# Kernel optimization log

Measured on AMD Instinct MI355X. Metric: run time of the kernel, lower is better.

## Reference

```python
import jax, jax.numpy as jnp
import numpy as np

SCALE = 10000.0
PSF = 21          # psf_h == psf_w == psf_d
PAD = PSF // 2    # 10


def setup_inputs() -> dict:
    key = jax.random.key(0)
    k1, k2, k3, k4, k5, k6, k7 = jax.random.split(key, 7)
    N = 8192
    BS, C, H, W, D = 1, 16, 256, 256, 64
    return {
        "psf_raw": jax.random.normal(k1, (N, 1, PSF, PSF, PSF), dtype=jnp.float32),
        "i_val": jax.random.uniform(k2, (N,), dtype=jnp.float32),
        "b": jax.random.randint(k3, (N,), 0, BS, dtype=jnp.int32),
        "ch": jax.random.randint(k4, (N,), 0, C, dtype=jnp.int32),
        "z": jax.random.randint(k5, (N,), 0, H, dtype=jnp.int32),
        "y": jax.random.randint(k6, (N,), 0, W, dtype=jnp.int32),
        "x": jax.random.randint(k7, (N,), 0, D, dtype=jnp.int32),
        "BS": BS, "C": C, "H": H, "W": W, "D": D,
    }


def reference(psf_raw, i_val, b, ch, z, y, x, BS, C, H, W, D):
    # 1) clamp_min_(psf, 0)
    psf = jnp.maximum(psf_raw, 0.0)
    # 2) normalize by per-emitter max over spatial dims
    psf = psf / psf.max(axis=(2, 3, 4), keepdims=True)
    # 3) scale by clamped intensity
    psf = psf * jnp.maximum(i_val, 0.0)[:, None, None, None, None]
    # 4) reshape (N, 1, p, p, p) -> (N, p, p, p) as in _place_psf
    psf = psf.reshape(-1, PSF, PSF, PSF)

    # scatter-add each patch into the padded volume; slice start in the padded
    # array is exactly the original coordinate (z_idx - pad == z).
    Hp, Wp, Dp = H + 2 * PAD, W + 2 * PAD, D + 2 * PAD
    iz = jnp.arange(PSF, dtype=jnp.int32)[:, None, None]   # (p,1,1)
    iy = jnp.arange(PSF, dtype=jnp.int32)[None, :, None]   # (1,p,1)
    ix = jnp.arange(PSF, dtype=jnp.int32)[None, None, :]   # (1,1,p)
    off = b * C + ch                                        # (N,)
    lin = (((off[:, None, None, None] * Hp + (z[:, None, None, None] + iz)) * Wp
            + (y[:, None, None, None] + iy)) * Dp
           + (x[:, None, None, None] + ix))                 # (N,p,p,p)

    flat = jnp.zeros(BS * C * Hp * Wp * Dp, dtype=psf.dtype)
    flat = flat.at[lin.reshape(-1)].add(psf.reshape(-1))
    vol = flat.reshape(BS, C, Hp, Wp, Dp)
    xsim = vol[:, :, PAD:PAD + H, PAD:PAD + W, PAD:PAD + D]
    return SCALE * xsim
```

## Files before the change

### kernel.cpp

```cpp
#include <hip/hip_runtime.h>
#include <hip/hip_fp16.h>

#define SCALE_F 10000.0f
#define PSF 21
#define PAD 10
#define PSF3 9261
#define PSF3P 9280
#define NTILES 16384
#define CAP 64

typedef float f32x4 __attribute__((ext_vector_type(4)));

#define META_OFF 0
#define CNT_OFF  131072
#define SCAN_OFF 196608
#define CUR_OFF  262144
#define LIST_OFF 327680
#define PSC_OFF  4521984

template<bool F16>
__global__ __launch_bounds__(256) void psf_scale_fill_kernel(
    const float* __restrict__ psf_raw,
    const float* __restrict__ i_val,
    const int* __restrict__ bArr, const int* __restrict__ chArr,
    const int* __restrict__ zArr, const int* __restrict__ yArr,
    const int* __restrict__ xArr,
    int4* __restrict__ meta,
    int*  __restrict__ cnt,
    int*  __restrict__ list,
    int cap,
    __half* __restrict__ pscaled)
{
    const int n   = blockIdx.x;
    const int tid = threadIdx.x;
    const float* p = psf_raw + (size_t)n * PSF3;

    const int peel = (4 - (n & 3)) & 3;
    const f32x4* p4 = (const f32x4*)(p + peel);
    const int nq  = (PSF3 - peel) >> 2;
    const int rem = (PSF3 - peel) & 3;

    float head = 0.0f, tailv = 0.0f;
    if (tid < peel) head  = p[tid];
    if (tid < rem)  tailv = p[PSF3 - rem + tid];

    f32x4 q[10];
    float m = fmaxf(fmaxf(head, tailv), 0.0f);
#pragma unroll
    for (int j = 0; j < 10; ++j) {
        const int k = tid + (j << 8);
        if (j < 9 || k < nq) {
            f32x4 v = __builtin_nontemporal_load(p4 + k);
            q[j] = v;
            m = fmaxf(m, fmaxf(fmaxf(v.x, v.y), fmaxf(v.z, v.w)));
        } else {
            q[j] = (f32x4)(0.0f);
        }
    }

#pragma unroll
    for (int off = 32; off > 0; off >>= 1)
        m = fmaxf(m, __shfl_down(m, off, 64));

    __shared__ float smax[4];
    if ((tid & 63) == 0) smax[tid >> 6] = m;
    __syncthreads();
    const float mm = fmaxf(fmaxf(smax[0], smax[1]), fmaxf(smax[2], smax[3]));
    const float sc = (mm > 0.0f) ? SCALE_F * fmaxf(i_val[n], 0.0f) / mm : 0.0f;

    if (F16) {
        __half* pb = pscaled + (size_t)n * PSF3P;
        if (tid < peel)
            pb[tid - peel] = __float2half_rn(sc * fmaxf(head, 0.0f));
        if (tid < rem)
            pb[PSF3 - rem + tid - peel] = __float2half_rn(sc * fmaxf(tailv, 0.0f));
        ushort4* pq = (ushort4*)pb;
#pragma unroll
        for (int j = 0; j < 10; ++j) {
            const int k = tid + (j << 8);
            if (j < 9 || k < nq) {
                ushort4 u;
                u.x = __half_as_ushort(__float2half_rn(sc * fmaxf(q[j].x, 0.0f)));
                u.y = __half_as_ushort(__float2half_rn(sc * fmaxf(q[j].y, 0.0f)));
                u.z = __half_as_ushort(__float2half_rn(sc * fmaxf(q[j].z, 0.0f)));
                u.w = __half_as_ushort(__float2half_rn(sc * fmaxf(q[j].w, 0.0f)));
                pq[k] = u;
            }
        }
    }

    if (tid == 0) {
        int z0 = zArr[n] - PAD, y0 = yArr[n] - PAD, x0 = xArr[n] - PAD;
        meta[n] = make_int4(z0, y0, x0, __float_as_int(sc));
        int c = bArr[n] * 16 + chArr[n];
        int tzlo = max(z0, 0) >> 3, tzhi = min(z0 + 20, 255) >> 3;
        int tylo = max(y0, 0) >> 3, tyhi = min(y0 + 20, 255) >> 3;
        if (cap > 0) {
            for (int tz = tzlo; tz <= tzhi; ++tz)
                for (int ty = tylo; ty <= tyhi; ++ty) {
                    int t = c * 1024 + tz * 32 + ty;
                    int pos = atomicAdd(&cnt[t], 1);
                    if (pos < cap) list[t * cap + pos] = n;
                }
        } else {
            for (int tz = tzlo; tz <= tzhi; ++tz)
                for (int ty = tylo; ty <= tyhi; ++ty)
                    atomicAdd(&cnt[c * 1024 + tz * 32 + ty], 1);
        }
    }
}

__global__ __launch_bounds__(256) void scan_kernel(
    const int4* __restrict__ cnt4, int4* __restrict__ off4, int4* __restrict__ cur4)
{
    const int t = threadIdx.x;
    int4 v[16];
#pragma unroll
    for (int i = 0; i < 16; ++i) v[i] = cnt4[t * 16 + i];
    int sum = 0;
#pragma unroll
    for (int i = 0; i < 16; ++i) sum += v[i].x + v[i].y + v[i].z + v[i].w;

    const int lane = t & 63, w = t >> 6;
    int s = sum;
#pragma unroll
    for (int d = 1; d < 64; d <<= 1) {
        int u = __shfl_up(s, d, 64);
        if (lane >= d) s += u;
    }
    __shared__ int wsum[4];
    if (lane == 63) wsum[w] = s;
    __syncthreads();
    int base = 0;
    for (int i = 0; i < w; ++i) base += wsum[i];
    int run = base + s - sum;

#pragma unroll
    for (int i = 0; i < 16; ++i) {
        int4 o;
        o.x = run; run += v[i].x;
        o.y = run; run += v[i].y;
        o.z = run; run += v[i].z;
        o.w = run; run += v[i].w;
        off4[t * 16 + i] = o;
        cur4[t * 16 + i] = o;
    }
}

__global__ __launch_bounds__(256) void fill_kernel(
    const int* __restrict__ bArr, const int* __restrict__ chArr,
    const int* __restrict__ zArr, const int* __restrict__ yArr,
    int* __restrict__ cursor, int* __restrict__ list, int N)
{
    int n = blockIdx.x * 256 + threadIdx.x;
    if (n >= N) return;
    int c = bArr[n] * 16 + chArr[n];
    int z0 = zArr[n] - PAD, y0 = yArr[n] - PAD;
    int tzlo = max(z0, 0) >> 3, tzhi = min(z0 + 20, 255) >> 3;
    int tylo = max(y0, 0) >> 3, tyhi = min(y0 + 20, 255) >> 3;
    for (int tz = tzlo; tz <= tzhi; ++tz)
        for (int ty = tylo; ty <= tyhi; ++ty) {
            int pos = atomicAdd(&cursor[c * 1024 + tz * 32 + ty], 1);
            list[pos] = n;
        }
}

template<bool F16>
__global__ __launch_bounds__(256) void gather_kernel(
    const float* __restrict__ psf_raw,
    const __half* __restrict__ pscaled,
    const int4* __restrict__ meta,
    const int* __restrict__ off, const int* __restrict__ cnt,
    const int* __restrict__ list,
    float* __restrict__ out,
    int cap)
{
    const int tile = blockIdx.x;
    const int ty = tile & 31;
    const int tz = (tile >> 5) & 31;
    const int c  = tile >> 10;
    const int t  = threadIdx.x;
    const int x    = t & 63;
    const int ysub = t >> 6;
    const int zbase = tz * 8;
    const int ybase = ty * 8;

    float acc0[8] = {};
    float acc1[8] = {};

    int o, cn;
    if (cap > 0) { o = tile * cap; cn = min(cnt[tile], cap); }
    else         { o = off[tile];  cn = cnt[tile]; }

    int  nnext = (cn > 0) ? list[o] : 0;
    int4 mnext = (cn > 0) ? meta[nnext] : make_int4(0, 0, 0, 0);

    for (int i = 0; i < cn; ++i) {
        const int  n  = __builtin_amdgcn_readfirstlane(nnext);
        const int4 mt = mnext;
        const int  nj = list[o + min(i + 1, cn - 1)];
        nnext = nj;
        mnext = meta[nj];

        const int z0 = __builtin_amdgcn_readfirstlane(mt.x);
        const int y0 = __builtin_amdgcn_readfirstlane(mt.y);
        const int x0 = __builtin_amdgcn_readfirstlane(mt.z);
        const float sc = __int_as_float(__builtin_amdgcn_readfirstlane(mt.w));

        const int dx  = x - x0;
        const float wsc = ((unsigned)dx < 21u) ? (F16 ? 1.0f : sc) : 0.0f;
        const int dxc = min(max(dx, 0), 20);

        const int dy0 = ybase + ysub - y0;
        const int dy1 = dy0 + 4;
        const int a0 = __any((unsigned)dy0 < 21u);
        const int a1 = __any((unsigned)dy1 < 21u);
        const int row0 = dy0 * 21 + dxc;
        const int row1 = dy1 * 21 + dxc;

        const float*  pbf = psf_raw + (size_t)n * PSF3;
        const __half* pbh = pscaled + (size_t)n * PSF3P - ((4 - (n & 3)) & 3);

        if (a0 & a1) {
#pragma unroll
            for (int zi = 0; zi < 8; ++zi) {
                const int dz = zbase + zi - z0;
                const int zo = min(max(dz, 0), 20) * 441;
                const float w = ((unsigned)dz < 21u) ? wsc : 0.0f;
                float v0 = F16 ? __half2float(pbh[zo + row0]) : fmaxf(pbf[zo + row0], 0.0f);
                float v1 = F16 ? __half2float(pbh[zo + row1]) : fmaxf(pbf[zo + row1], 0.0f);
                acc0[zi] += w * v0;
                acc1[zi] += w * v1;
            }
        } else if (a0) {
#pragma unroll
            for (int zi = 0; zi < 8; ++zi) {
                const int dz = zbase + zi - z0;
                const int zo = min(max(dz, 0), 20) * 441;
                const float w = ((unsigned)dz < 21u) ? wsc : 0.0f;
                float v0 = F16 ? __half2float(pbh[zo + row0]) : fmaxf(pbf[zo + row0], 0.0f);
                acc0[zi] += w * v0;
            }
        } else if (a1) {
#pragma unroll
            for (int zi = 0; zi < 8; ++zi) {
                const int dz = zbase + zi - z0;
                const int zo = min(max(dz, 0), 20) * 441;
                const float w = ((unsigned)dz < 21u) ? wsc : 0.0f;
                float v1 = F16 ? __half2float(pbh[zo + row1]) : fmaxf(pbf[zo + row1], 0.0f);
                acc1[zi] += w * v1;
            }
        }
    }

    const size_t outbase = (((size_t)c * 256 + zbase) * 256 + ybase) * 64 + x;
#pragma unroll
    for (int zi = 0; zi < 8; ++zi) {
        __builtin_nontemporal_store(acc0[zi],
            &out[outbase + (size_t)zi * (256 * 64) + (size_t)ysub * 64]);
        __builtin_nontemporal_store(acc1[zi],
            &out[outbase + (size_t)zi * (256 * 64) + (size_t)(ysub + 4) * 64]);
    }
}

extern "C" void kernel_launch(void* const* d_in, const int* in_sizes, int n_in,
                              void* d_out, int out_size, void* d_ws, size_t ws_size,
                              hipStream_t stream) {
    const float* psf_raw = (const float*)d_in[0];
    const float* i_val   = (const float*)d_in[1];
    const int*   bArr    = (const int*)d_in[2];
    const int*   chArr   = (const int*)d_in[3];
    const int*   zArr    = (const int*)d_in[4];
    const int*   yArr    = (const int*)d_in[5];
    const int*   xArr    = (const int*)d_in[6];
    float* out = (float*)d_out;

    const int N = in_sizes[1];

    char* ws = (char*)d_ws;
    int4*   meta    = (int4*)(ws + META_OFF);
    int*    cnt     = (int*)(ws + CNT_OFF);
    int*    offp    = (int*)(ws + SCAN_OFF);
    int*    cursor  = (int*)(ws + CUR_OFF);
    int*    list    = (int*)(ws + LIST_OFF);
    __half* pscaled = (__half*)(ws + PSC_OFF) + 16;

    const size_t psc_need = (size_t)PSC_OFF + 64 + (size_t)N * PSF3P * 2;
    bool f16 = (ws_size >= psc_need);
    int cap;
    if (ws_size >= (size_t)LIST_OFF + (size_t)CAP * NTILES * 4) {
        cap = CAP;
    } else {
        size_t avail = (ws_size > LIST_OFF) ? ws_size - LIST_OFF : 0;
        size_t cap_s = avail / ((size_t)NTILES * sizeof(int));
        cap = (cap_s >= 24) ? (int)((cap_s < 64) ? cap_s : 64) : 0;
    }
    if (cap == 0) f16 = false;

    (void)hipMemsetAsync(cnt, 0, NTILES * sizeof(int), stream);

    if (f16)
        psf_scale_fill_kernel<true><<<N, 256, 0, stream>>>(psf_raw, i_val, bArr, chArr,
            zArr, yArr, xArr, meta, cnt, list, cap, pscaled);
    else
        psf_scale_fill_kernel<false><<<N, 256, 0, stream>>>(psf_raw, i_val, bArr, chArr,
            zArr, yArr, xArr, meta, cnt, list, cap, pscaled);

    if (cap == 0) {
        scan_kernel<<<1, 256, 0, stream>>>((const int4*)cnt, (int4*)offp, (int4*)cursor);
        fill_kernel<<<(N + 255) / 256, 256, 0, stream>>>(bArr, chArr, zArr, yArr,
                                                         cursor, list, N);
    }

    if (f16)
        gather_kernel<true><<<NTILES, 256, 0, stream>>>(psf_raw, pscaled, meta,
            offp, cnt, list, out, cap);
    else
        gather_kernel<false><<<NTILES, 256, 0, stream>>>(psf_raw, pscaled, meta,
            offp, cnt, list, out, cap);
}
```

Before: 168.3 us.

## Pre-shift fp16 PSF rows to even alignment for paired half2 gather loads

The prep kernel now stages each scaled fp16 PSF in LDS and rewrites it into a padded layout with 22-element rows, shifted by the parity of the emitter's x origin. The gather kernel can then have each thread handle two adjacent x outputs with one aligned half2 load per z slice and write float2 stores, halving per-element load instructions. Costs: extra LDS staging and index division in the prep kernel, a slightly larger scratch buffer, and the f16 path now assumes the fixed CAP without checking that the workspace holds the list.

```diff
diff --git a/kernel.cpp b/kernel.cpp
--- a/kernel.cpp
+++ b/kernel.cpp
@@ -5,11 +5,15 @@
 #define PSF 21
 #define PAD 10
 #define PSF3 9261
-#define PSF3P 9280
+#define ROWP 22
+#define ZSTR 462
+#define PSFP 9704
+#define NQUAD 2426
 #define NTILES 16384
 #define CAP 64
 
 typedef float f32x4 __attribute__((ext_vector_type(4)));
+typedef float f32x2 __attribute__((ext_vector_type(2)));
 
 #define META_OFF 0
 #define CNT_OFF  131072
@@ -18,8 +22,7 @@
 #define LIST_OFF 327680
 #define PSC_OFF  4521984
 
-template<bool F16>
-__global__ __launch_bounds__(256) void psf_scale_fill_kernel(
+__global__ __launch_bounds__(256) void psf_scale_fill_f16(
     const float* __restrict__ psf_raw,
     const float* __restrict__ i_val,
     const int* __restrict__ bArr, const int* __restrict__ chArr,
@@ -28,7 +31,6 @@
     int4* __restrict__ meta,
     int*  __restrict__ cnt,
     int*  __restrict__ list,
-    int cap,
     __half* __restrict__ pscaled)
 {
     const int n   = blockIdx.x;
@@ -63,50 +65,183 @@
         m = fmaxf(m, __shfl_down(m, off, 64));
 
     __shared__ float smax[4];
+    __shared__ unsigned short lds[PSF3];
     if ((tid & 63) == 0) smax[tid >> 6] = m;
     __syncthreads();
     const float mm = fmaxf(fmaxf(smax[0], smax[1]), fmaxf(smax[2], smax[3]));
     const float sc = (mm > 0.0f) ? SCALE_F * fmaxf(i_val[n], 0.0f) / mm : 0.0f;
 
-    if (F16) {
-        __half* pb = pscaled + (size_t)n * PSF3P;
-        if (tid < peel)
-            pb[tid - peel] = __float2half_rn(sc * fmaxf(head, 0.0f));
-        if (tid < rem)
-            pb[PSF3 - rem + tid - peel] = __float2half_rn(sc * fmaxf(tailv, 0.0f));
-        ushort4* pq = (ushort4*)pb;
-#pragma unroll
-        for (int j = 0; j < 10; ++j) {
-            const int k = tid + (j << 8);
-            if (j < 9 || k < nq) {
-                ushort4 u;
-                u.x = __half_as_ushort(__float2half_rn(sc * fmaxf(q[j].x, 0.0f)));
-                u.y = __half_as_ushort(__float2half_rn(sc * fmaxf(q[j].y, 0.0f)));
-                u.z = __half_as_ushort(__float2half_rn(sc * fmaxf(q[j].z, 0.0f)));
-                u.w = __half_as_ushort(__float2half_rn(sc * fmaxf(q[j].w, 0.0f)));
-                pq[k] = u;
-            }
+    if (tid < peel)
+        lds[tid] = __half_as_ushort(__float2half_rn(sc * fmaxf(head, 0.0f)));
+    if (tid < rem)
+        lds[PSF3 - rem + tid] = __half_as_ushort(__float2half_rn(sc * fmaxf(tailv, 0.0f)));
+#pragma unroll
+    for (int j = 0; j < 10; ++j) {
+        const int k = tid + (j << 8);
+        if (j < 9 || k < nq) {
+            const int base = peel + (k << 2);
+            lds[base + 0] = __half_as_ushort(__float2half_rn(sc * fmaxf(q[j].x, 0.0f)));
+            lds[base + 1] = __half_as_ushort(__float2half_rn(sc * fmaxf(q[j].y, 0.0f)));
+            lds[base + 2] = __half_as_ushort(__float2half_rn(sc * fmaxf(q[j].z, 0.0f)));
+            lds[base + 3] = __half_as_ushort(__float2half_rn(sc * fmaxf(q[j].w, 0.0f)));
+        }
+    }
+    __syncthreads();
+
+    const int x0 = xArr[n] - PAD;
+    const int s  = x0 & 1;
+    ushort4* outp = (ushort4*)(pscaled + (size_t)n * PSFP);
+#pragma unroll
+    for (int it = 0; it < 10; ++it) {
+        const int q4 = tid + (it << 8);
+        if (it < 9 || q4 < NQUAD) {
+            const int o0 = q4 << 2;
+            ushort4 u;
+#pragma unroll
+            for (int cc = 0; cc < 4; ++cc) {
+                const int o   = o0 + cc;
+                const int row = o / ROWP;
+                const int j   = o - row * ROWP;
+                const int px  = j - s;
+                unsigned short val = 0;
+                if ((unsigned)px < 21u && row < 441)
+                    val = lds[row * 21 + px];
+                (&u.x)[cc] = val;
+            }
+            outp[q4] = u;
         }
     }
 
     if (tid == 0) {
+        int z0 = zArr[n] - PAD, y0 = yArr[n] - PAD;
+        meta[n] = make_int4(z0, y0, x0, __float_as_int(sc));
+        int c = bArr[n] * 16 + chArr[n];
+        int tzlo = max(z0, 0) >> 3, tzhi = min(z0 + 20, 255) >> 3;
+        int tylo = max(y0, 0) >> 3, tyhi = min(y0 + 20, 255) >> 3;
+        for (int tz = tzlo; tz <= tzhi; ++tz)
+            for (int ty = tylo; ty <= tyhi; ++ty) {
+                int t = c * 1024 + tz * 32 + ty;
+                int pos = atomicAdd(&cnt[t], 1);
+                if (pos < CAP) list[t * CAP + pos] = n;
+            }
+    }
+}
+
+__global__ __launch_bounds__(256) void gather_f16(
+    const __half* __restrict__ pscaled,
+    const int4* __restrict__ meta,
+    const int* __restrict__ cnt,
+    const int* __restrict__ list,
+    float* __restrict__ out)
+{
+    const int b  = blockIdx.x;
+    const int ty = b & 31;
+    const int tz = (b >> 5) & 31;
+    const int c  = b >> 10;
+    const int tile = b;
+
+    const int t    = threadIdx.x;
+    const int xp   = t & 31;
+    const int yrow = t >> 5;
+    const int zbase = tz * 8;
+    const int ybase = ty * 8;
+
+    float acc0[8] = {};
+    float acc1[8] = {};
+
+    const int o  = tile * CAP;
+    const int cn = min(cnt[tile], CAP);
+
+    int  nnext = (cn > 0) ? list[o] : 0;
+    int4 mnext = (cn > 0) ? meta[nnext] : make_int4(0, 0, 0, 0);
+
+    for (int i = 0; i < cn; ++i) {
+        const int  n  = __builtin_amdgcn_readfirstlane(nnext);
+        const int4 mt = mnext;
+        const int  nj = list[o + min(i + 1, cn - 1)];
+        nnext = nj;
+        mnext = meta[nj];
+
+        const int z0 = __builtin_amdgcn_readfirstlane(mt.x);
+        const int y0 = __builtin_amdgcn_readfirstlane(mt.y);
+        const int x0 = __builtin_amdgcn_readfirstlane(mt.z);
+        const int x0e = x0 & ~1;
+
+        const int dy = ybase + yrow - y0;
+        if (!__any((unsigned)dy < 21u)) continue;
+
+        const int dxs = 2 * xp - x0e;
+        const bool wy  = (unsigned)dy < 21u;
+        const float wxy0 = (wy && (unsigned)dxs       < 22u) ? 1.0f : 0.0f;
+        const float wxy1 = (wy && (unsigned)(dxs + 1) < 22u) ? 1.0f : 0.0f;
+
+        const int dxsc = min(max(dxs, 0), 20);
+        const int rowoff = min(max(dy, 0), 20) * ROWP + dxsc;
+        const __half* pb = pscaled + (size_t)n * PSFP;
+
+#pragma unroll
+        for (int zi = 0; zi < 8; ++zi) {
+            const int dz = zbase + zi - z0;
+            const int zo = min(max(dz, 0), 20) * ZSTR;
+            const bool okz = (unsigned)dz < 21u;
+            const __half2 hv = *reinterpret_cast<const __half2*>(pb + zo + rowoff);
+            const float2 f = __half22float2(hv);
+            const float w0 = okz ? wxy0 : 0.0f;
+            const float w1 = okz ? wxy1 : 0.0f;
+            acc0[zi] += w0 * f.x;
+            acc1[zi] += w1 * f.y;
+        }
+    }
+
+    const size_t outbase = (((size_t)c * 256 + zbase) * 256 + ybase + yrow) * 64 + 2 * xp;
+#pragma unroll
+    for (int zi = 0; zi < 8; ++zi) {
+        f32x2 v; v.x = acc0[zi]; v.y = acc1[zi];
+        __builtin_nontemporal_store(v,
+            (f32x2*)(out + outbase + (size_t)zi * (256 * 64)));
+    }
+}
+
+__global__ __launch_bounds__(256) void psf_scale_fill_f32(
+    const float* __restrict__ psf_raw,
+    const float* __restrict__ i_val,
+    const int* __restrict__ bArr, const int* __restrict__ chArr,
+    const int* __restrict__ zArr, const int* __restrict__ yArr,
+    const int* __restrict__ xArr,
+    int4* __restrict__ meta,
+    int*  __restrict__ cnt,
+    int*  __restrict__ list,
+    int cap)
+{
+    const int n   = blockIdx.x;
+    const int tid = threadIdx.x;
+    const float* p = psf_raw + (size_t)n * PSF3;
+    float m = 0.0f;
+    for (int k = tid; k < PSF3; k += 256) m = fmaxf(m, p[k]);
+#pragma unroll
+    for (int off = 32; off > 0; off >>= 1)
+        m = fmaxf(m, __shfl_down(m, off, 64));
+    __shared__ float smax[4];
+    if ((tid & 63) == 0) smax[tid >> 6] = m;
+    __syncthreads();
+    if (tid == 0) {
+        float mm = fmaxf(fmaxf(smax[0], smax[1]), fmaxf(smax[2], smax[3]));
+        float sc = (mm > 0.0f) ? SCALE_F * fmaxf(i_val[n], 0.0f) / mm : 0.0f;
         int z0 = zArr[n] - PAD, y0 = yArr[n] - PAD, x0 = xArr[n] - PAD;
         meta[n] = make_int4(z0, y0, x0, __float_as_int(sc));
         int c = bArr[n] * 16 + chArr[n];
         int tzlo = max(z0, 0) >> 3, tzhi = min(z0 + 20, 255) >> 3;
         int tylo = max(y0, 0) >> 3, tyhi = min(y0 + 20, 255) >> 3;
-        if (cap > 0) {
-            for (int tz = tzlo; tz <= tzhi; ++tz)
-                for (int ty = tylo; ty <= tyhi; ++ty) {
-                    int t = c * 1024 + tz * 32 + ty;
+        for (int tz = tzlo; tz <= tzhi; ++tz)
+            for (int ty = tylo; ty <= tyhi; ++ty) {
+                int t = c * 1024 + tz * 32 + ty;
+                if (cap > 0) {
                     int pos = atomicAdd(&cnt[t], 1);
                     if (pos < cap) list[t * cap + pos] = n;
+                } else {
+                    atomicAdd(&cnt[t], 1);
                 }
-        } else {
-            for (int tz = tzlo; tz <= tzhi; ++tz)
-                for (int ty = tylo; ty <= tyhi; ++ty)
-                    atomicAdd(&cnt[c * 1024 + tz * 32 + ty], 1);
-        }
+            }
     }
 }
 
@@ -120,7 +255,6 @@
     int sum = 0;
 #pragma unroll
     for (int i = 0; i < 16; ++i) sum += v[i].x + v[i].y + v[i].z + v[i].w;
-
     const int lane = t & 63, w = t >> 6;
     int s = sum;
 #pragma unroll
@@ -134,16 +268,15 @@
     int base = 0;
     for (int i = 0; i < w; ++i) base += wsum[i];
     int run = base + s - sum;
-
 #pragma unroll
     for (int i = 0; i < 16; ++i) {
-        int4 o;
-        o.x = run; run += v[i].x;
-        o.y = run; run += v[i].y;
-        o.z = run; run += v[i].z;
-        o.w = run; run += v[i].w;
-        off4[t * 16 + i] = o;
-        cur4[t * 16 + i] = o;
+        int4 oo;
+        oo.x = run; run += v[i].x;
+        oo.y = run; run += v[i].y;
+        oo.z = run; run += v[i].z;
+        oo.w = run; run += v[i].w;
+        off4[t * 16 + i] = oo;
+        cur4[t * 16 + i] = oo;
     }
 }
 
@@ -165,10 +298,8 @@
         }
 }
 
-template<bool F16>
-__global__ __launch_bounds__(256) void gather_kernel(
+__global__ __launch_bounds__(256) void gather_f32(
     const float* __restrict__ psf_raw,
-    const __half* __restrict__ pscaled,
     const int4* __restrict__ meta,
     const int* __restrict__ off, const int* __restrict__ cnt,
     const int* __restrict__ list,
@@ -208,18 +339,16 @@
         const float sc = __int_as_float(__builtin_amdgcn_readfirstlane(mt.w));
 
         const int dx  = x - x0;
-        const float wsc = ((unsigned)dx < 21u) ? (F16 ? 1.0f : sc) : 0.0f;
+        const float wsc = ((unsigned)dx < 21u) ? sc : 0.0f;
         const int dxc = min(max(dx, 0), 20);
 
         const int dy0 = ybase + ysub - y0;
         const int dy1 = dy0 + 4;
         const int a0 = __any((unsigned)dy0 < 21u);
         const int a1 = __any((unsigned)dy1 < 21u);
-        const int row0 = dy0 * 21 + dxc;
-        const int row1 = dy1 * 21 + dxc;
-
-        const float*  pbf = psf_raw + (size_t)n * PSF3;
-        const __half* pbh = pscaled + (size_t)n * PSF3P - ((4 - (n & 3)) & 3);
+        const int row0 = min(max(dy0, 0), 20) * 21 + dxc;
+        const int row1 = min(max(dy1, 0), 20) * 21 + dxc;
+        const float* pb = psf_raw + (size_t)n * PSF3;
 
         if (a0 & a1) {
 #pragma unroll
@@ -227,10 +356,8 @@
                 const int dz = zbase + zi - z0;
                 const int zo = min(max(dz, 0), 20) * 441;
                 const float w = ((unsigned)dz < 21u) ? wsc : 0.0f;
-                float v0 = F16 ? __half2float(pbh[zo + row0]) : fmaxf(pbf[zo + row0], 0.0f);
-                float v1 = F16 ? __half2float(pbh[zo + row1]) : fmaxf(pbf[zo + row1], 0.0f);
-                acc0[zi] += w * v0;
-                acc1[zi] += w * v1;
+                acc0[zi] += w * fmaxf(pb[zo + row0], 0.0f);
+                acc1[zi] += w * fmaxf(pb[zo + row1], 0.0f);
             }
         } else if (a0) {
 #pragma unroll
@@ -238,8 +365,7 @@
                 const int dz = zbase + zi - z0;
                 const int zo = min(max(dz, 0), 20) * 441;
                 const float w = ((unsigned)dz < 21u) ? wsc : 0.0f;
-                float v0 = F16 ? __half2float(pbh[zo + row0]) : fmaxf(pbf[zo + row0], 0.0f);
-                acc0[zi] += w * v0;
+                acc0[zi] += w * fmaxf(pb[zo + row0], 0.0f);
             }
         } else if (a1) {
 #pragma unroll
@@ -247,8 +373,7 @@
                 const int dz = zbase + zi - z0;
                 const int zo = min(max(dz, 0), 20) * 441;
                 const float w = ((unsigned)dz < 21u) ? wsc : 0.0f;
-                float v1 = F16 ? __half2float(pbh[zo + row1]) : fmaxf(pbf[zo + row1], 0.0f);
-                acc1[zi] += w * v1;
+                acc1[zi] += w * fmaxf(pb[zo + row1], 0.0f);
             }
         }
     }
@@ -283,39 +408,33 @@
     int*    offp    = (int*)(ws + SCAN_OFF);
     int*    cursor  = (int*)(ws + CUR_OFF);
     int*    list    = (int*)(ws + LIST_OFF);
-    __half* pscaled = (__half*)(ws + PSC_OFF) + 16;
-
-    const size_t psc_need = (size_t)PSC_OFF + 64 + (size_t)N * PSF3P * 2;
-    bool f16 = (ws_size >= psc_need);
-    int cap;
-    if (ws_size >= (size_t)LIST_OFF + (size_t)CAP * NTILES * 4) {
-        cap = CAP;
+    __half* pscaled = (__half*)(ws + PSC_OFF);
+
+    const size_t f16_need = (size_t)PSC_OFF + (size_t)N * PSFP * 2;
+    const bool f16 = (ws_size >= f16_need);
+
+    (void)hipMemsetAsync(cnt, 0, NTILES * sizeof(int), stream);
+
+    if (f16) {
+        psf_scale_fill_f16<<<N, 256, 0, stream>>>(psf_raw, i_val, bArr, chArr,
+            zArr, yArr, xArr, meta, cnt, list, pscaled);
+        gather_f16<<<NTILES, 256, 0, stream>>>(pscaled, meta, cnt, list, out);
     } else {
-        size_t avail = (ws_size > LIST_OFF) ? ws_size - LIST_OFF : 0;
-        size_t cap_s = avail / ((size_t)NTILES * sizeof(int));
-        cap = (cap_s >= 24) ? (int)((cap_s < 64) ? cap_s : 64) : 0;
-    }
-    if (cap == 0) f16 = false;
-
-    (void)hipMemsetAsync(cnt, 0, NTILES * sizeof(int), stream);
-
-    if (f16)
-        psf_scale_fill_kernel<true><<<N, 256, 0, stream>>>(psf_raw, i_val, bArr, chArr,
-            zArr, yArr, xArr, meta, cnt, list, cap, pscaled);
-    else
-        psf_scale_fill_kernel<false><<<N, 256, 0, stream>>>(psf_raw, i_val, bArr, chArr,
-            zArr, yArr, xArr, meta, cnt, list, cap, pscaled);
-
-    if (cap == 0) {
-        scan_kernel<<<1, 256, 0, stream>>>((const int4*)cnt, (int4*)offp, (int4*)cursor);
-        fill_kernel<<<(N + 255) / 256, 256, 0, stream>>>(bArr, chArr, zArr, yArr,
-                                                         cursor, list, N);
-    }
-
-    if (f16)
-        gather_kernel<true><<<NTILES, 256, 0, stream>>>(psf_raw, pscaled, meta,
-            offp, cnt, list, out, cap);
-    else
-        gather_kernel<false><<<NTILES, 256, 0, stream>>>(psf_raw, pscaled, meta,
-            offp, cnt, list, out, cap);
-}
+        int cap;
+        if (ws_size >= (size_t)LIST_OFF + (size_t)CAP * NTILES * 4) {
+            cap = CAP;
+        } else {
+            size_t avail = (ws_size > LIST_OFF) ? ws_size - LIST_OFF : 0;
+            size_t cap_s = avail / ((size_t)NTILES * sizeof(int));
+            cap = (cap_s >= 24) ? (int)((cap_s < 64) ? cap_s : 64) : 0;
+        }
+        psf_scale_fill_f32<<<N, 256, 0, stream>>>(psf_raw, i_val, bArr, chArr,
+            zArr, yArr, xArr, meta, cnt, list, cap);
+        if (cap == 0) {
+            scan_kernel<<<1, 256, 0, stream>>>((const int4*)cnt, (int4*)offp, (int4*)cursor);
+            fill_kernel<<<(N + 255) / 256, 256, 0, stream>>>(bArr, chArr, zArr, yArr,
+                                                             cursor, list, N);
+        }
+        gather_f32<<<NTILES, 256, 0, stream>>>(psf_raw, meta, offp, cnt, list, out, cap);
+    }
+}
```

Measured after the change: 188.6 us. 1.12x slower.
